# Performance work log

Hardware: AMD Instinct MI355X
Metric: run time of the kernel (lower is better)

## Reference

```python
import jax, jax.numpy as jnp
import numpy as np

B, T, IN, H, L = 256, 1024, 21, 30, 5
G = 4 * H  # gate dim, PyTorch gate order: i, f, g, o


def _run_dir(xs, h0, c0, Wih, Whh, b, reverse):
    # xs: [T, B, F]; returns hidden sequence [T, B, H] in original time order
    xs2 = xs[::-1] if reverse else xs

    def step(carry, xt):
        h, c = carry
        g = xt @ Wih.T + h @ Whh.T + b  # [B, 4H]
        i, f, gg, o = jnp.split(g, 4, axis=-1)
        c = jax.nn.sigmoid(f) * c + jax.nn.sigmoid(i) * jnp.tanh(gg)
        h = jax.nn.sigmoid(o) * jnp.tanh(c)
        return (h, c), h

    _, hs = jax.lax.scan(step, (h0, c0), xs2)
    return hs[::-1] if reverse else hs


def _stack_bilstm(xs, wih_list, whh, b, h0, c0):
    # xs: [T, B, F]; wih_list[l]: [2, 4H, in_l]; whh/b: [L, 2, ...]; h0/c0: [L, 2, B, H]
    for l in range(L):
        fwd = _run_dir(xs, h0[l, 0], c0[l, 0], wih_list[l][0], whh[l, 0], b[l, 0], False)
        bwd = _run_dir(xs, h0[l, 1], c0[l, 1], wih_list[l][1], whh[l, 1], b[l, 1], True)
        xs = jnp.concatenate([fwd, bwd], axis=-1)  # [T, B, 2H]
    return xs


def setup_inputs() -> dict:
    key = jax.random.key(0)
    ks = jax.random.split(key, 14)
    s = jnp.float32(0.1)
    f32 = jnp.float32
    return {
        "x": jax.random.normal(ks[0], (B, T, IN), f32),
        "w_ih1_l0": jax.random.normal(ks[1], (2, G, IN), f32) * s,
        "w_ih1_rest": jax.random.normal(ks[2], (L - 1, 2, G, 2 * H), f32) * s,
        "w_hh1": jax.random.normal(ks[3], (L, 2, G, H), f32) * s,
        "b1": jax.random.normal(ks[4], (L, 2, G), f32) * s,
        "w_ih2": jax.random.normal(ks[5], (L, 2, G, 2 * H), f32) * s,
        "w_hh2": jax.random.normal(ks[6], (L, 2, G, H), f32) * s,
        "b2": jax.random.normal(ks[7], (L, 2, G), f32) * s,
        "h01": jax.random.normal(ks[8], (2 * L, B, H), f32) * s,
        "c01": jax.random.normal(ks[9], (2 * L, B, H), f32) * s,
        "h02": jax.random.normal(ks[10], (2 * L, B, H), f32) * s,
        "c02": jax.random.normal(ks[11], (2 * L, B, H), f32) * s,
        "fc_w": jax.random.normal(ks[12], (2, 2 * H), f32) * s,
        "fc_b": jax.random.normal(ks[13], (2,), f32) * s,
    }


def reference(x, w_ih1_l0, w_ih1_rest, w_hh1, b1, w_ih2, w_hh2, b2,
              h01, c01, h02, c02, fc_w, fc_b):
    xs = jnp.transpose(x, (1, 0, 2))  # [T, B, IN]
    # PyTorch packs hidden as [num_layers*num_dirs, B, H] with index layer*2+dir
    h01r = h01.reshape(L, 2, B, H); c01r = c01.reshape(L, 2, B, H)
    h02r = h02.reshape(L, 2, B, H); c02r = c02.reshape(L, 2, B, H)
    wih1 = [w_ih1_l0] + [w_ih1_rest[i] for i in range(L - 1)]
    xs = _stack_bilstm(xs, wih1, w_hh1, b1, h01r, c01r)
    wih2 = [w_ih2[i] for i in range(L)]
    xs = _stack_bilstm(xs, wih2, w_hh2, b2, h02r, c02r)
    last = xs[-1]  # out[:, -1, :] -> [B, 2H]
    # dropout is identity in eval mode
    return jnp.tanh(last @ fc_w.T + fc_b)
```

## Files before the change

kernel.cpp:

```cpp
#include <hip/hip_runtime.h>

#define T_LEN 1024
#define BATCH 256
#define HID   30

__device__ __forceinline__ float ftanh(float x) {
    x = fminf(fmaxf(x, -15.0f), 15.0f);
    float e = __expf(2.0f * x);
    return (e - 1.0f) / (e + 1.0f);
}

__device__ __forceinline__ float rl(float v, int srclane) {
    return __int_as_float(__builtin_amdgcn_readlane(__float_as_int(v), srclane));
}

template<int IN_L>
__global__ __attribute__((amdgpu_waves_per_eu(1, 1))) __launch_bounds__(64)
void lstm_wave(const float* __restrict__ in,
               float* __restrict__ out,
               const float* __restrict__ wih,
               const float* __restrict__ whh,
               const float* __restrict__ bias,
               const float* __restrict__ h0,
               const float* __restrict__ c0)
{
    constexpr int WS    = 8;
    constexpr int NW    = T_LEN / WS;
    constexpr int ELEMS = WS * IN_L;
    constexpr int NLOAD = (ELEMS + 63) / 64;

    const int b = blockIdx.x, d = blockIdx.y, lane = threadIdx.x;

    __shared__ float xt[2][ELEMS];

    const int rowA = (lane < 60) ? lane : 59;
    float wA[IN_L + HID], wB[IN_L + HID];
    {
        const float* ra = wih + (size_t)(d * 120 + rowA) * IN_L;
        const float* rb = ra + 60 * IN_L;
        #pragma unroll
        for (int k = 0; k < IN_L; k++) { wA[k] = ra[k]; wB[k] = rb[k]; }
        const float* ha = whh + (size_t)(d * 120 + rowA) * HID;
        const float* hb = ha + 60 * HID;
        #pragma unroll
        for (int k = 0; k < HID; k++) { wA[IN_L + k] = ha[k]; wB[IN_L + k] = hb[k]; }
    }
    float bA = bias[d * 120 + rowA];
    float bB = bias[d * 120 + 60 + rowA];

    #pragma unroll
    for (int k = 0; k < IN_L + HID; k++) {
        asm volatile("" : "+v"(wA[k]));
        asm volatile("" : "+v"(wB[k]));
    }
    asm volatile("" : "+v"(bA));
    asm volatile("" : "+v"(bB));

    float hval = 0.f, cval = 0.f;
    {
        int j = (lane < HID) ? lane : 0;
        float hl = h0[(size_t)(d * BATCH + b) * HID + j];
        float cl = c0[(size_t)(d * BATCH + b) * HID + j];
        if (lane < HID) { hval = hl; cval = cl; }
    }

    const int t0 = d ? (T_LEN - 1) : 0;
    const int ts = d ? -1 : 1;
    const float* xin = in + (size_t)b * T_LEN * IN_L;
    float* outp = out + (size_t)b * T_LEN * 60 + (size_t)t0 * 60 + d * HID
                      + ((lane < HID) ? lane : 0);

    const float km  = (lane < HID) ? 2.f : 1.f;
    const float kba = (lane < HID) ? 2.f : 1.f;
    const float kbb = (lane < HID) ? -1.f : 0.f;

    float xg[NLOAD];

    auto stage_load = [&](int w) {
        const float* base = xin + (size_t)(t0 + ts * (WS * w)) * IN_L;
        #pragma unroll
        for (int r = 0; r < NLOAD; r++) {
            int e = r * 64 + lane;
            if (e < ELEMS) xg[r] = base[ts * (e / IN_L) * IN_L + (e % IN_L)];
        }
    };
    auto stage_write = [&](int buf) {
        asm volatile("s_waitcnt lgkmcnt(0)" ::: "memory");
        #pragma unroll
        for (int r = 0; r < NLOAD; r++) {
            int e = r * 64 + lane;
            if (e < ELEMS) xt[buf][e] = xg[r];
        }
        asm volatile("s_waitcnt lgkmcnt(0)" ::: "memory");
        __builtin_amdgcn_sched_barrier(0);
    };

    stage_load(0);
    stage_write(0);

    for (int w = 0; w < NW; ++w) {
        if (w + 1 < NW) stage_load(w + 1);
        const float* xb = xt[w & 1];
        #pragma unroll 2
        for (int s = 0; s < WS; ++s) {
            float aA0 = bA, aA1 = 0.f, aB0 = bB, aB1 = 0.f;
            const float* xr = xb + s * IN_L;
            #pragma unroll
            for (int k = 0; k + 1 < IN_L; k += 2) {
                float x0 = xr[k], x1 = xr[k + 1];
                aA0 += wA[k] * x0;     aB0 += wB[k] * x0;
                aA1 += wA[k + 1] * x1; aB1 += wB[k + 1] * x1;
            }
            if constexpr (IN_L & 1) {
                float x0 = xr[IN_L - 1];
                aA0 += wA[IN_L - 1] * x0; aB0 += wB[IN_L - 1] * x0;
            }
            #pragma unroll
            for (int k = 0; k < HID; k += 2) {
                float h0v = rl(hval, k), h1v = rl(hval, k + 1);
                aA0 += wA[IN_L + k] * h0v;     aB0 += wB[IN_L + k] * h0v;
                aA1 += wA[IN_L + k + 1] * h1v; aB1 += wB[IN_L + k + 1] * h1v;
            }
            float aA = aA0 + aA1, aB = aB0 + aB1;

            float sA = __builtin_amdgcn_rcpf(1.f + __expf(-aA));
            float sB = __builtin_amdgcn_rcpf(1.f + __expf(-(km * aB)));
            sB = kba * sB + kbb;

            float sf = __shfl(sA, lane + 30, 64);
            float so = __shfl(sB, lane + 30, 64);

            cval = sf * cval + sA * sB;
            float tc = 2.f * __builtin_amdgcn_rcpf(1.f + __expf(-2.f * cval)) - 1.f;
            float hn = so * tc;
            hval = hn;

            if (lane < HID) *outp = hn;
            outp += ts * 60;
        }
        if (w + 1 < NW) stage_write((w + 1) & 1);
    }
}

__global__ void fc_kernel(const float* __restrict__ hbuf,
                          const float* __restrict__ fc_w,
                          const float* __restrict__ fc_b,
                          float* __restrict__ out)
{
    int b = threadIdx.x;
    if (b < BATCH) {
        const float* h = hbuf + ((size_t)b * T_LEN + (T_LEN - 1)) * 60;
        #pragma unroll
        for (int j = 0; j < 2; j++) {
            float acc = fc_b[j];
            #pragma unroll
            for (int k = 0; k < 60; k++) acc += fc_w[j * 60 + k] * h[k];
            out[b * 2 + j] = ftanh(acc);
        }
    }
}

extern "C" void kernel_launch(void* const* d_in, const int* in_sizes, int n_in,
                              void* d_out, int out_size, void* d_ws, size_t ws_size,
                              hipStream_t stream) {
    const float* x          = (const float*)d_in[0];
    const float* w_ih1_l0   = (const float*)d_in[1];
    const float* w_ih1_rest = (const float*)d_in[2];
    const float* w_hh1      = (const float*)d_in[3];
    const float* b1         = (const float*)d_in[4];
    const float* w_ih2      = (const float*)d_in[5];
    const float* w_hh2      = (const float*)d_in[6];
    const float* b2         = (const float*)d_in[7];
    const float* h01        = (const float*)d_in[8];
    const float* c01        = (const float*)d_in[9];
    const float* h02        = (const float*)d_in[10];
    const float* c02        = (const float*)d_in[11];
    const float* fc_w       = (const float*)d_in[12];
    const float* fc_b       = (const float*)d_in[13];
    float* out = (float*)d_out;

    float* bufA = (float*)d_ws;
    float* bufB = bufA + (size_t)BATCH * T_LEN * 60;

    dim3 grid(BATCH, 2), blk(64);

    lstm_wave<21><<<grid, blk, 0, stream>>>(x, bufA,
        w_ih1_l0, w_hh1, b1, h01, c01);
    const float* curb = bufA;
    float*       nxtb = bufB;
    for (int l = 1; l < 5; l++) {
        lstm_wave<60><<<grid, blk, 0, stream>>>(curb, nxtb,
            w_ih1_rest + (size_t)(l - 1) * 2 * 120 * 60,
            w_hh1      + (size_t)l * 2 * 120 * HID,
            b1         + (size_t)l * 2 * 120,
            h01        + (size_t)l * 2 * BATCH * HID,
            c01        + (size_t)l * 2 * BATCH * HID);
        float* tmp = (float*)curb; curb = nxtb; nxtb = tmp;
    }
    for (int l = 0; l < 5; l++) {
        lstm_wave<60><<<grid, blk, 0, stream>>>(curb, nxtb,
            w_ih2 + (size_t)l * 2 * 120 * 60,
            w_hh2 + (size_t)l * 2 * 120 * HID,
            b2    + (size_t)l * 2 * 120,
            h02   + (size_t)l * 2 * BATCH * HID,
            c02   + (size_t)l * 2 * BATCH * HID);
        float* tmp = (float*)curb; curb = nxtb; nxtb = tmp;
    }

    fc_kernel<<<1, 256, 0, stream>>>(curb, fc_w, fc_b, out);
}
```

Before: 5.847 ms.

## Move input weights to LDS and drop single-wave occupancy limit

Input-projection weights now live in shared memory as interleaved float4 tiles instead of per-lane registers. Inputs are padded to a multiple of four so the dot product uses vector LDS reads, and the step loop is fully unrolled. Removing the waves_per_eu(1,1) attribute and the register-pinning asm lowers VGPR pressure, so more waves can share a SIMD. The cost is extra LDS traffic on the serial per-step critical path, plus a larger shared footprint per block.

Result: slower. 9.321 ms (+59.4%).

```diff
diff --git a/kernel.cpp b/kernel.cpp
--- a/kernel.cpp
+++ b/kernel.cpp
@@ -15,7 +15,7 @@
 }
 
 template<int IN_L>
-__global__ __attribute__((amdgpu_waves_per_eu(1, 1))) __launch_bounds__(64)
+__global__ __launch_bounds__(64)
 void lstm_wave(const float* __restrict__ in,
                float* __restrict__ out,
                const float* __restrict__ wih,
@@ -24,37 +24,42 @@
                const float* __restrict__ h0,
                const float* __restrict__ c0)
 {
+    constexpr int IN_P  = (IN_L + 3) & ~3;
     constexpr int WS    = 8;
     constexpr int NW    = T_LEN / WS;
-    constexpr int ELEMS = WS * IN_L;
-    constexpr int NLOAD = (ELEMS + 63) / 64;
+    constexpr int XELE  = WS * IN_L;
+    constexpr int NLOAD = (XELE + 63) / 64;
+    constexpr int NQ    = IN_P / 4;
 
     const int b = blockIdx.x, d = blockIdx.y, lane = threadIdx.x;
 
-    __shared__ float xt[2][ELEMS];
+    __shared__ __align__(16) float wlds[120 * IN_P];
+    __shared__ __align__(16) float xt[2][WS * IN_P];
 
     const int rowA = (lane < 60) ? lane : 59;
-    float wA[IN_L + HID], wB[IN_L + HID];
+
+    float whA[HID], whB[HID];
     {
-        const float* ra = wih + (size_t)(d * 120 + rowA) * IN_L;
-        const float* rb = ra + 60 * IN_L;
-        #pragma unroll
-        for (int k = 0; k < IN_L; k++) { wA[k] = ra[k]; wB[k] = rb[k]; }
         const float* ha = whh + (size_t)(d * 120 + rowA) * HID;
         const float* hb = ha + 60 * HID;
         #pragma unroll
-        for (int k = 0; k < HID; k++) { wA[IN_L + k] = ha[k]; wB[IN_L + k] = hb[k]; }
+        for (int k = 0; k < HID; k++) { whA[k] = ha[k]; whB[k] = hb[k]; }
     }
     float bA = bias[d * 120 + rowA];
     float bB = bias[d * 120 + 60 + rowA];
 
-    #pragma unroll
-    for (int k = 0; k < IN_L + HID; k++) {
-        asm volatile("" : "+v"(wA[k]));
-        asm volatile("" : "+v"(wB[k]));
-    }
-    asm volatile("" : "+v"(bA));
-    asm volatile("" : "+v"(bB));
+    for (int e = lane; e < 120 * IN_P; e += 64) {
+        int row = e / IN_P, k = e % IN_P;
+        float v = (k < IN_L) ? wih[(size_t)(d * 120 + row) * IN_L + k] : 0.f;
+        wlds[(k >> 2) * 480 + row * 4 + (k & 3)] = v;
+    }
+    if constexpr (IN_P > IN_L) {
+        constexpr int NPAD = IN_P - IN_L;
+        for (int e = lane; e < 2 * WS * NPAD; e += 64) {
+            int buf = e / (WS * NPAD), r = e % (WS * NPAD);
+            xt[buf][(r / NPAD) * IN_P + IN_L + (r % NPAD)] = 0.f;
+        }
+    }
 
     float hval = 0.f, cval = 0.f;
     {
@@ -81,7 +86,7 @@
         #pragma unroll
         for (int r = 0; r < NLOAD; r++) {
             int e = r * 64 + lane;
-            if (e < ELEMS) xg[r] = base[ts * (e / IN_L) * IN_L + (e % IN_L)];
+            if (e < XELE) xg[r] = base[ts * (e / IN_L) * IN_L + (e % IN_L)];
         }
     };
     auto stage_write = [&](int buf) {
@@ -89,7 +94,7 @@
         #pragma unroll
         for (int r = 0; r < NLOAD; r++) {
             int e = r * 64 + lane;
-            if (e < ELEMS) xt[buf][e] = xg[r];
+            if (e < XELE) xt[buf][(e / IN_L) * IN_P + (e % IN_L)] = xg[r];
         }
         asm volatile("s_waitcnt lgkmcnt(0)" ::: "memory");
         __builtin_amdgcn_sched_barrier(0);
@@ -101,25 +106,24 @@
     for (int w = 0; w < NW; ++w) {
         if (w + 1 < NW) stage_load(w + 1);
         const float* xb = xt[w & 1];
-        #pragma unroll 2
+        #pragma unroll
         for (int s = 0; s < WS; ++s) {
             float aA0 = bA, aA1 = 0.f, aB0 = bB, aB1 = 0.f;
-            const float* xr = xb + s * IN_L;
             #pragma unroll
-            for (int k = 0; k + 1 < IN_L; k += 2) {
-                float x0 = xr[k], x1 = xr[k + 1];
-                aA0 += wA[k] * x0;     aB0 += wB[k] * x0;
-                aA1 += wA[k + 1] * x1; aB1 += wB[k + 1] * x1;
-            }
-            if constexpr (IN_L & 1) {
-                float x0 = xr[IN_L - 1];
-                aA0 += wA[IN_L - 1] * x0; aB0 += wB[IN_L - 1] * x0;
+            for (int q = 0; q < NQ; q++) {
+                float4 xv = *(const float4*)&xb[s * IN_P + q * 4];
+                float4 wa = *(const float4*)&wlds[q * 480 + rowA * 4];
+                float4 wb = *(const float4*)&wlds[q * 480 + rowA * 4 + 240];
+                aA0 += wa.x * xv.x; aA1 += wa.y * xv.y;
+                aA0 += wa.z * xv.z; aA1 += wa.w * xv.w;
+                aB0 += wb.x * xv.x; aB1 += wb.y * xv.y;
+                aB0 += wb.z * xv.z; aB1 += wb.w * xv.w;
             }
             #pragma unroll
             for (int k = 0; k < HID; k += 2) {
                 float h0v = rl(hval, k), h1v = rl(hval, k + 1);
-                aA0 += wA[IN_L + k] * h0v;     aB0 += wB[IN_L + k] * h0v;
-                aA1 += wA[IN_L + k + 1] * h1v; aB1 += wB[IN_L + k + 1] * h1v;
+                aA0 += whA[k] * h0v;     aB0 += whB[k] * h0v;
+                aA1 += whA[k + 1] * h1v; aB1 += whB[k + 1] * h1v;
             }
             float aA = aA0 + aA1, aB = aB0 + aB1;
 
```
